# Optimization experiments

Measured on AMD Instinct MI355X. Metric: run time of the kernel, lower is better.

## Reference

```python
import jax, jax.numpy as jnp
import numpy as np

K_SPARSE = 64  # number of units kept active per row

def setup_inputs() -> dict:
    key = jax.random.key(0)
    x = jax.random.normal(key, (16384, 4096), dtype=jnp.float32)
    return {"x": x}

def reference(x) -> jnp.ndarray:
    # Training-phase path of KSparse.call -> k_sparsify:
    # kth_smallest = sort(x)[..., n-1-k]  (the (k+1)-th largest value per row)
    # out = x * (x > kth_smallest)
    n = x.shape[-1]
    sorted_x = jnp.sort(x, axis=-1)              # ascending, [B, D]
    kth = sorted_x[:, n - 1 - K_SPARSE]          # [B]
    mask = (x > kth[:, None]).astype(x.dtype)    # strictly greater, as in source
    return x * mask
```

## Files before the change

kernel.cpp:

```cpp
#include <hip/hip_runtime.h>

#define K_SPARSE 64
#define COLS     4096
#define NTHREADS 256
#define EPT      (COLS / NTHREADS)
#define VPT      (EPT / 4)
#define LIST_CAP 4104

typedef float    nfloat4 __attribute__((ext_vector_type(4)));
typedef unsigned nuint4  __attribute__((ext_vector_type(4)));

__device__ __forceinline__ unsigned mapf(unsigned b) {
    return (b & 0x80000000u) ? ~b : (b | 0x80000000u);
}
__device__ __forceinline__ float unmapf(unsigned u) {
    unsigned b = (u & 0x80000000u) ? (u ^ 0x80000000u) : ~u;
    return __uint_as_float(b);
}

__global__ __launch_bounds__(NTHREADS)
void ksparse_select(const float* __restrict__ x, float* __restrict__ out, int rows)
{
    const int row = blockIdx.x;
    if (row >= rows) return;
    const int t    = threadIdx.x;
    const int lane = t & 63;
    const int w    = t >> 6;

    __shared__ __align__(16) unsigned list[LIST_CAP];
    __shared__ unsigned wtot[4];
    __shared__ unsigned s_kth;

    const float4* __restrict__ xrow =
        reinterpret_cast<const float4*>(x) + (size_t)row * (COLS / 4);
    nfloat4* __restrict__ orow =
        reinterpret_cast<nfloat4*>(out) + (size_t)row * (COLS / 4);

    float4   cur[VPT];
    unsigned u[EPT];
#pragma unroll
    for (int i = 0; i < VPT; ++i) cur[i] = xrow[t + i * NTHREADS];
#pragma unroll
    for (int i = 0; i < VPT; ++i) {
        u[i * 4 + 0] = mapf(__float_as_uint(cur[i].x));
        u[i * 4 + 1] = mapf(__float_as_uint(cur[i].y));
        u[i * 4 + 2] = mapf(__float_as_uint(cur[i].z));
        u[i * 4 + 3] = mapf(__float_as_uint(cur[i].w));
    }

    unsigned uT = 0, cnt = 0, base = 0, c = 0;
    for (int r = 0; r < 4; ++r) {
        uT = (r == 0) ? 0xBFF33333u
           : (r == 1) ? 0xBF666666u
           : (r == 2) ? 0x00800000u : 0u;
        cnt = 0;
#pragma unroll
        for (int i = 0; i < EPT; ++i) cnt += (u[i] > uT) ? 1u : 0u;

        unsigned s = cnt;
#pragma unroll
        for (int off = 1; off < 64; off <<= 1) {
            unsigned v = __shfl_up(s, off, 64);
            if (lane >= off) s += v;
        }
        if (lane == 63) wtot[w] = s;
        __syncthreads();
        const unsigned c0 = wtot[0], c1 = wtot[1], c2 = wtot[2], c3 = wtot[3];
        c = c0 + c1 + c2 + c3;
        if (c >= K_SPARSE + 1 || r == 3) {
            unsigned wbase = (w > 0 ? c0 : 0u) + (w > 1 ? c1 : 0u) + (w > 2 ? c2 : 0u);
            base = wbase + s - cnt;
            break;
        }
        __syncthreads();
    }

    unsigned pos = base;
#pragma unroll
    for (int i = 0; i < EPT; ++i) {
        if (u[i] > uT) list[pos++] = u[i];
    }
    if (t < 8) list[c + t] = 0u;
    __syncthreads();

    const int nq = (int)((c + 3) >> 2);
    const nuint4* listv = reinterpret_cast<const nuint4*>(list);
    for (int j = t; j < (int)c; j += NTHREADS) {
        const unsigned vj = list[j];
        unsigned g = 0, e = 0;
        for (int q = 0; q < nq; ++q) {
            const nuint4 ql = listv[q];
            g += (ql.x > vj) + (ql.y > vj) + (ql.z > vj) + (ql.w > vj);
            e += (ql.x == vj) + (ql.y == vj) + (ql.z == vj) + (ql.w == vj);
        }
        if (g <= (unsigned)K_SPARSE && (unsigned)K_SPARSE < g + e)
            s_kth = vj;
    }
    __syncthreads();

    const float kth = unmapf(s_kth);

#pragma unroll
    for (int i = 0; i < VPT; ++i) {
        nfloat4 o;
        o.x = (cur[i].x > kth) ? cur[i].x : 0.0f;
        o.y = (cur[i].y > kth) ? cur[i].y : 0.0f;
        o.z = (cur[i].z > kth) ? cur[i].z : 0.0f;
        o.w = (cur[i].w > kth) ? cur[i].w : 0.0f;
        __builtin_nontemporal_store(o, &orow[t + i * NTHREADS]);
    }
}

extern "C" void kernel_launch(void* const* d_in, const int* in_sizes, int n_in,
                              void* d_out, int out_size, void* d_ws, size_t ws_size,
                              hipStream_t stream) {
    const float* x = (const float*)d_in[0];
    float* out = (float*)d_out;
    const int rows = in_sizes[0] / COLS;
    ksparse_select<<<rows, NTHREADS, 0, stream>>>(x, out, rows);
}
```

Before: 74.20 us.

## Halve block size, drop float copy, shrink LDS list with radix fallback

```diff
diff --git a/kernel.cpp b/kernel.cpp
--- a/kernel.cpp
+++ b/kernel.cpp
@@ -2,10 +2,11 @@
 
 #define K_SPARSE 64
 #define COLS     4096
-#define NTHREADS 256
+#define NTHREADS 128
 #define EPT      (COLS / NTHREADS)
 #define VPT      (EPT / 4)
-#define LIST_CAP 4104
+#define FAST_CAP 1024
+#define LIST_CAP (FAST_CAP + 8)
 
 typedef float    nfloat4 __attribute__((ext_vector_type(4)));
 typedef unsigned nuint4  __attribute__((ext_vector_type(4)));
@@ -18,7 +19,7 @@
     return __uint_as_float(b);
 }
 
-__global__ __launch_bounds__(NTHREADS)
+__global__ __launch_bounds__(NTHREADS, 8)
 void ksparse_select(const float* __restrict__ x, float* __restrict__ out, int rows)
 {
     const int row = blockIdx.x;
@@ -28,7 +29,7 @@
     const int w    = t >> 6;
 
     __shared__ __align__(16) unsigned list[LIST_CAP];
-    __shared__ unsigned wtot[4];
+    __shared__ unsigned wtot[2];
     __shared__ unsigned s_kth;
 
     const float4* __restrict__ xrow =
@@ -36,16 +37,14 @@
     nfloat4* __restrict__ orow =
         reinterpret_cast<nfloat4*>(out) + (size_t)row * (COLS / 4);
 
-    float4   cur[VPT];
     unsigned u[EPT];
 #pragma unroll
-    for (int i = 0; i < VPT; ++i) cur[i] = xrow[t + i * NTHREADS];
-#pragma unroll
     for (int i = 0; i < VPT; ++i) {
-        u[i * 4 + 0] = mapf(__float_as_uint(cur[i].x));
-        u[i * 4 + 1] = mapf(__float_as_uint(cur[i].y));
-        u[i * 4 + 2] = mapf(__float_as_uint(cur[i].z));
-        u[i * 4 + 3] = mapf(__float_as_uint(cur[i].w));
+        float4 v = xrow[t + i * NTHREADS];
+        u[i * 4 + 0] = mapf(__float_as_uint(v.x));
+        u[i * 4 + 1] = mapf(__float_as_uint(v.y));
+        u[i * 4 + 2] = mapf(__float_as_uint(v.z));
+        u[i * 4 + 3] = mapf(__float_as_uint(v.w));
     }
 
     unsigned uT = 0, cnt = 0, base = 0, c = 0;
@@ -65,48 +64,66 @@
         }
         if (lane == 63) wtot[w] = s;
         __syncthreads();
-        const unsigned c0 = wtot[0], c1 = wtot[1], c2 = wtot[2], c3 = wtot[3];
-        c = c0 + c1 + c2 + c3;
+        const unsigned c0 = wtot[0], c1 = wtot[1];
+        c = c0 + c1;
         if (c >= K_SPARSE + 1 || r == 3) {
-            unsigned wbase = (w > 0 ? c0 : 0u) + (w > 1 ? c1 : 0u) + (w > 2 ? c2 : 0u);
-            base = wbase + s - cnt;
+            base = (w > 0 ? c0 : 0u) + s - cnt;
             break;
         }
         __syncthreads();
     }
 
-    unsigned pos = base;
+    unsigned ukth;
+    if (c >= K_SPARSE + 1 && c <= FAST_CAP) {
+        unsigned pos = base;
 #pragma unroll
-    for (int i = 0; i < EPT; ++i) {
-        if (u[i] > uT) list[pos++] = u[i];
+        for (int i = 0; i < EPT; ++i) {
+            if (u[i] > uT) list[pos++] = u[i];
+        }
+        if (t < 8) list[c + t] = 0u;
+        __syncthreads();
+
+        const int nq = (int)((c + 3) >> 2);
+        const nuint4* listv = reinterpret_cast<const nuint4*>(list);
+        for (int j = t; j < (int)c; j += NTHREADS) {
+            const unsigned vj = list[j];
+            unsigned g = 0, e = 0;
+            for (int q = 0; q < nq; ++q) {
+                const nuint4 ql = listv[q];
+                g += (ql.x > vj) + (ql.y > vj) + (ql.z > vj) + (ql.w > vj);
+                e += (ql.x == vj) + (ql.y == vj) + (ql.z == vj) + (ql.w == vj);
+            }
+            if (g <= (unsigned)K_SPARSE && (unsigned)K_SPARSE < g + e)
+                s_kth = vj;
+        }
+        __syncthreads();
+        ukth = s_kth;
+    } else {
+        unsigned prefix = 0u;
+        for (int b = 31; b >= 0; --b) {
+            const unsigned trial = prefix | (1u << b);
+            unsigned c2 = 0;
+#pragma unroll
+            for (int i = 0; i < EPT; ++i) c2 += (u[i] >= trial) ? 1u : 0u;
+#pragma unroll
+            for (int off = 32; off >= 1; off >>= 1)
+                c2 += __shfl_xor(c2, off, 64);
+            if (lane == 0) wtot[w] = c2;
+            __syncthreads();
+            const unsigned tot = wtot[0] + wtot[1];
+            if (tot >= K_SPARSE + 1) prefix = trial;
+            __syncthreads();
+        }
+        ukth = prefix;
     }
-    if (t < 8) list[c + t] = 0u;
-    __syncthreads();
-
-    const int nq = (int)((c + 3) >> 2);
-    const nuint4* listv = reinterpret_cast<const nuint4*>(list);
-    for (int j = t; j < (int)c; j += NTHREADS) {
-        const unsigned vj = list[j];
-        unsigned g = 0, e = 0;
-        for (int q = 0; q < nq; ++q) {
-            const nuint4 ql = listv[q];
-            g += (ql.x > vj) + (ql.y > vj) + (ql.z > vj) + (ql.w > vj);
-            e += (ql.x == vj) + (ql.y == vj) + (ql.z == vj) + (ql.w == vj);
-        }
-        if (g <= (unsigned)K_SPARSE && (unsigned)K_SPARSE < g + e)
-            s_kth = vj;
-    }
-    __syncthreads();
-
-    const float kth = unmapf(s_kth);
 
 #pragma unroll
     for (int i = 0; i < VPT; ++i) {
         nfloat4 o;
-        o.x = (cur[i].x > kth) ? cur[i].x : 0.0f;
-        o.y = (cur[i].y > kth) ? cur[i].y : 0.0f;
-        o.z = (cur[i].z > kth) ? cur[i].z : 0.0f;
-        o.w = (cur[i].w > kth) ? cur[i].w : 0.0f;
+        o.x = (u[i * 4 + 0] > ukth) ? unmapf(u[i * 4 + 0]) : 0.0f;
+        o.y = (u[i * 4 + 1] > ukth) ? unmapf(u[i * 4 + 1]) : 0.0f;
+        o.z = (u[i * 4 + 2] > ukth) ? unmapf(u[i * 4 + 2]) : 0.0f;
+        o.w = (u[i * 4 + 3] > ukth) ? unmapf(u[i * 4 + 3]) : 0.0f;
         __builtin_nontemporal_store(o, &orow[t + i * NTHREADS]);
     }
 }
```

New measurement: 79.41 us. 7.0% more time.
